# Kernel tuning notes

Measured on AMD Instinct MI355X. Metric: run time of the kernel, lower is better.

## Reference

```python
import jax, jax.numpy as jnp
import numpy as np

N = 50000   # nodes
E = 800000  # edges (avg degree 16)
F_IN = 128
H = 128
L = 4
LN_EPS = 1e-5


def setup_inputs() -> dict:
    key = jax.random.key(0)
    ks = jax.random.split(key, 4)
    x = jax.random.normal(ks[0], (N, F_IN), dtype=jnp.float32)
    edge_index = jax.random.randint(ks[1], (2, E), 0, N)
    conv_w = jax.random.normal(ks[2], (L, F_IN, H), dtype=jnp.float32) * 0.05
    conv_b = jnp.zeros((L, H), dtype=jnp.float32)
    ln_g = jnp.ones((L, H), dtype=jnp.float32)
    ln_b = jnp.zeros((L, H), dtype=jnp.float32)
    head_w = jax.random.normal(ks[3], (H, 1), dtype=jnp.float32) * 0.05
    head_b = jnp.zeros((1,), dtype=jnp.float32)
    return {"x": x, "edge_index": edge_index, "conv_w": conv_w, "conv_b": conv_b,
            "ln_g": ln_g, "ln_b": ln_b, "head_w": head_w, "head_b": head_b}


def _layer_norm(h, g, b):
    mu = jnp.mean(h, axis=-1, keepdims=True)
    var = jnp.mean(jnp.square(h - mu), axis=-1, keepdims=True)
    return (h - mu) * jax.lax.rsqrt(var + LN_EPS) * g + b


def _gcn_conv(h, W, b, src, dst, inv_sqrt_deg, inv_deg):
    # PyG GCNConv: self-loops + symmetric normalization D^-1/2 (A+I) D^-1/2, then bias.
    hw = h @ W  # (N, H)
    norm = inv_sqrt_deg[src] * inv_sqrt_deg[dst]  # (E,)
    msg = hw[src] * norm[:, None]  # gather + edgewise scale
    agg = jax.ops.segment_sum(msg, dst, num_segments=N)  # scatter-add
    agg = agg + hw * inv_deg[:, None]  # self-loop term (norm = 1/deg)
    return agg + b


def reference(x, edge_index, conv_w, conv_b, ln_g, ln_b, head_w, head_b):
    src, dst = edge_index[0], edge_index[1]
    # degree on target nodes, including self-loop
    deg = jax.ops.segment_sum(jnp.ones((E,), x.dtype), dst, num_segments=N) + 1.0
    inv_sqrt_deg = jax.lax.rsqrt(deg)
    inv_deg = 1.0 / deg
    h = x
    for i in range(L):
        h = _gcn_conv(h, conv_w[i], conv_b[i], src, dst, inv_sqrt_deg, inv_deg)
        h = _layer_norm(h, ln_g[i], ln_b[i])
        if i != L - 1:
            h = jax.nn.gelu(h, approximate=False)
            # dropout is identity in eval mode
    scores = (h @ head_w + head_b).squeeze(-1)  # (N,)
    return scores, h
```

## Files before the change

### kernel.cpp

```cpp
#include <hip/hip_runtime.h>
#include <math.h>

#define N_NODES 50000
#define N_EDGES 800000
#define HDIM 128
#define NLAYERS 4
#define LN_EPS 1e-5f
#define EQUARTER (N_EDGES / 4)
#define SEG 64
#define FILLB ((EQUARTER + 255) / 256)
#define GEMMB ((N_NODES + 63) / 64)

typedef __attribute__((ext_vector_type(8))) short short8;
typedef __attribute__((ext_vector_type(4))) float floatx4;

__device__ __forceinline__ ushort f2bf(float x) {
    unsigned b = __float_as_uint(x);
    unsigned r = b + 0x7fffu + ((b >> 16) & 1u);
    return (ushort)(r >> 16);
}
__device__ __forceinline__ float2 bf2f2(unsigned u) {
    return make_float2(__uint_as_float(u << 16), __uint_as_float(u & 0xffff0000u));
}


__device__ __forceinline__ void fill_body(int bid, int tid, const int* __restrict__ src,
                                          const int* __restrict__ dst, int* __restrict__ cnt,
                                          ushort* __restrict__ csr16) {
    int t = bid * 256 + tid;
    if (t >= EQUARTER) return;
    int s0 = src[t],                d0 = dst[t];
    int s1 = src[t + EQUARTER],     d1 = dst[t + EQUARTER];
    int s2 = src[t + 2 * EQUARTER], d2 = dst[t + 2 * EQUARTER];
    int s3 = src[t + 3 * EQUARTER], d3 = dst[t + 3 * EQUARTER];
    int p0 = atomicAdd(&cnt[d0], 1);
    int p1 = atomicAdd(&cnt[d1], 1);
    int p2 = atomicAdd(&cnt[d2], 1);
    int p3 = atomicAdd(&cnt[d3], 1);
    if (p0 < SEG) csr16[d0 * SEG + p0] = (ushort)s0;
    if (p1 < SEG) csr16[d1 * SEG + p1] = (ushort)s1;
    if (p2 < SEG) csr16[d2 * SEG + p2] = (ushort)s2;
    if (p3 < SEG) csr16[d3 * SEG + p3] = (ushort)s3;
}

__global__ __launch_bounds__(256) void isd_kernel(const int* __restrict__ cnt,
                                                  float* __restrict__ isd,
                                                  float* __restrict__ ind) {
    int i = blockIdx.x * 256 + threadIdx.x;
    if (i < N_NODES) {
        float d = (float)cnt[i] + 1.0f;
        isd[i] = rsqrtf(d);
        ind[i] = 1.0f / d;
    }
}

__global__ __launch_bounds__(256) void bprep_kernel(const float* __restrict__ W,
                                                    ushort* __restrict__ bfrag) {
    int idx = blockIdx.x * 256 + threadIdx.x;
    if (idx >= NLAYERS * 4 * 8 * 64) return;
    int lane = idx & 63;
    int t = (idx >> 6) & 7;
    int s = (idx >> 9) & 3;
    int l = idx >> 11;
    int n = t * 16 + (lane & 15);
    int kb = s * 32 + (lane >> 4) * 8;
    const float* Wl = W + (size_t)l * HDIM * HDIM;
    union { uint4 q; ushort u[8]; } o;
#pragma unroll
    for (int j = 0; j < 8; ++j) o.u[j] = f2bf(Wl[(size_t)(kb + j) * HDIM + n]);
    *(uint4*)&bfrag[(size_t)idx * 8] = o.q;
}

template <bool A_FP32>
__device__ __forceinline__ void gemm_body(int bid, int tid, const void* __restrict__ Av,
                                          const ushort* __restrict__ bfrag,
                                          ushort* __restrict__ out) {
    int wave = tid >> 6, lane = tid & 63;
    int quad = lane >> 4, mrow = lane & 15;
    int rowBase = bid * 64 + wave * 16;
    int arow = rowBase + mrow;
    bool aok = arow < N_NODES;

    floatx4 acc[8];
#pragma unroll
    for (int t = 0; t < 8; ++t) acc[t] = (floatx4)0.f;

#pragma unroll
    for (int s = 0; s < 4; ++s) {
        union { short8 v; ushort u[8]; } af;
        if (A_FP32) {
            const float* A = (const float*)Av;
            if (aok) {
                const float* p = &A[(size_t)arow * HDIM + s * 32 + quad * 8];
#pragma unroll
                for (int j = 0; j < 8; ++j) af.u[j] = f2bf(p[j]);
            } else {
#pragma unroll
                for (int j = 0; j < 8; ++j) af.u[j] = 0;
            }
        } else {
            const ushort* A = (const ushort*)Av;
            if (aok) {
                af.v = *(const short8*)&A[(size_t)arow * HDIM + s * 32 + quad * 8];
            } else {
#pragma unroll
                for (int j = 0; j < 8; ++j) af.u[j] = 0;
            }
        }
#pragma unroll
        for (int t = 0; t < 8; ++t) {
            short8 bf = *(const short8*)&bfrag[(size_t)(((s * 8 + t) * 64) + lane) * 8];
            acc[t] = __builtin_amdgcn_mfma_f32_16x16x32_bf16(af.v, bf, acc[t], 0, 0, 0);
        }
    }
#pragma unroll
    for (int t = 0; t < 8; ++t) {
#pragma unroll
        for (int r = 0; r < 4; ++r) {
            int row = rowBase + quad * 4 + r;
            if (row < N_NODES) out[(size_t)row * HDIM + t * 16 + mrow] = f2bf(acc[t][r]);
        }
    }
}

__global__ __launch_bounds__(256) void fused0_kernel(
    const int* __restrict__ src, const int* __restrict__ dst, int* __restrict__ cnt,
    ushort* __restrict__ csr16, const float* __restrict__ x,
    const ushort* __restrict__ bfrag0, ushort* __restrict__ hw) {
    if (blockIdx.x < FILLB)
        fill_body(blockIdx.x, threadIdx.x, src, dst, cnt, csr16);
    else
        gemm_body<true>(blockIdx.x - FILLB, threadIdx.x, x, bfrag0, hw);
}

__global__ __launch_bounds__(256) void gemm_mfma_kernel(const ushort* __restrict__ A,
                                                        const ushort* __restrict__ bfrag,
                                                        ushort* __restrict__ out) {
    gemm_body<false>(blockIdx.x, threadIdx.x, A, bfrag, out);
}

__global__ __launch_bounds__(256) void agg_ln_kernel(
    const uint2* __restrict__ hw2, const int* __restrict__ degcnt,
    const ushort* __restrict__ csr16, const float* __restrict__ isd,
    const float* __restrict__ ind, const float* __restrict__ conv_b,
    const float* __restrict__ ln_g, const float* __restrict__ ln_b,
    uint2* __restrict__ hout_bf, float* __restrict__ hout_f32,
    const float* __restrict__ head_w, const float* __restrict__ head_b,
    float* __restrict__ scores, int final_layer) {
    int wave = threadIdx.x >> 6;
    int lane = threadIdx.x & 63;
    int g = lane >> 5;
    int li = lane & 31;
    int n = blockIdx.x * 4 + wave;
    if (n >= N_NODES) return;
    int c = li * 4;

    float isd_n = isd[n], ind_n = ind[n];
    int rs = n * SEG;
    int deg = min(degcnt[n], SEG);

    float e0 = 0.f, e1 = 0.f, e2 = 0.f, e3 = 0.f;
    int sj = 0;
    float wj = 0.f;
    if (lane < deg) {
        sj = (int)csr16[rs + lane];
        wj = isd[sj];
    }
    for (int j = 0; j < deg; j += 8) {
#pragma unroll
        for (int t = 0; t < 4; ++t) {
            int idx = j + 2 * t + g;
            int s = __shfl(sj, idx);
            float w = __shfl(wj, idx);
            uint2 u = hw2[(size_t)s * 32 + li];
            float2 q0 = bf2f2(u.x), q1 = bf2f2(u.y);
            e0 = fmaf(q0.x, w, e0); e1 = fmaf(q0.y, w, e1);
            e2 = fmaf(q1.x, w, e2); e3 = fmaf(q1.y, w, e3);
        }
    }
    e0 += __shfl_xor(e0, 32); e1 += __shfl_xor(e1, 32);
    e2 += __shfl_xor(e2, 32); e3 += __shfl_xor(e3, 32);

    uint2 hv = hw2[(size_t)n * 32 + li];
    float2 h0 = bf2f2(hv.x), h1 = bf2f2(hv.y);
    float4 cb = *(const float4*)&conv_b[c];
    float a0 = fmaf(e0, isd_n, fmaf(h0.x, ind_n, cb.x));
    float a1 = fmaf(e1, isd_n, fmaf(h0.y, ind_n, cb.y));
    float a2 = fmaf(e2, isd_n, fmaf(h1.x, ind_n, cb.z));
    float a3 = fmaf(e3, isd_n, fmaf(h1.y, ind_n, cb.w));

    float sum = a0 + a1 + a2 + a3;
#pragma unroll
    for (int o = 1; o < 32; o <<= 1) sum += __shfl_xor(sum, o);
    float mu = sum * (1.0f / HDIM);
    float d0 = a0 - mu, d1 = a1 - mu, d2 = a2 - mu, d3 = a3 - mu;
    float vs = d0 * d0 + d1 * d1 + d2 * d2 + d3 * d3;
#pragma unroll
    for (int o = 1; o < 32; o <<= 1) vs += __shfl_xor(vs, o);
    float rstd = rsqrtf(vs * (1.0f / HDIM) + LN_EPS);
    float4 gv = *(const float4*)&ln_g[c];
    float4 bv = *(const float4*)&ln_b[c];
    float y0 = fmaf(d0 * rstd, gv.x, bv.x);
    float y1 = fmaf(d1 * rstd, gv.y, bv.y);
    float y2 = fmaf(d2 * rstd, gv.z, bv.z);
    float y3 = fmaf(d3 * rstd, gv.w, bv.w);

    if (!final_layer) {
#define GELU(v) ((v) = 0.5f * (v) * (1.0f + erff((v) * 0.70710678118654752f)))
        GELU(y0); GELU(y1); GELU(y2); GELU(y3);
#undef GELU
        if (g == 0) {
            uint2 ov;
            ov.x = (unsigned)f2bf(y0) | ((unsigned)f2bf(y1) << 16);
            ov.y = (unsigned)f2bf(y2) | ((unsigned)f2bf(y3) << 16);
            hout_bf[(size_t)n * 32 + li] = ov;
        }
    } else {
        if (g == 0)
            *(float4*)&hout_f32[(size_t)n * HDIM + c] = make_float4(y0, y1, y2, y3);
        float4 hwv = *(const float4*)&head_w[c];
        float p = y0 * hwv.x + y1 * hwv.y + y2 * hwv.z + y3 * hwv.w;
#pragma unroll
        for (int o = 1; o < 32; o <<= 1) p += __shfl_xor(p, o);
        if (lane == 0) scores[n] = p + head_b[0];
    }
}


extern "C" void kernel_launch(void* const* d_in, const int* in_sizes, int n_in,
                              void* d_out, int out_size, void* d_ws, size_t ws_size,
                              hipStream_t stream) {
    const float* x      = (const float*)d_in[0];
    const int*   eidx   = (const int*)d_in[1];
    const float* conv_w = (const float*)d_in[2];
    const float* conv_b = (const float*)d_in[3];
    const float* ln_g   = (const float*)d_in[4];
    const float* ln_b   = (const float*)d_in[5];
    const float* head_w = (const float*)d_in[6];
    const float* head_b = (const float*)d_in[7];
    float* out = (float*)d_out;

    const int* src = eidx;
    const int* dst = eidx + N_EDGES;

    char* ws = (char*)d_ws;
    size_t o = 0;
    auto alloc = [&](size_t elems) {
        void* p = ws + o * 4;
        o += (elems + 15) & ~(size_t)15;
        return p;
    };
    int*      cnt      = (int*)alloc(N_NODES);
    float*    isd      = (float*)alloc(N_NODES);
    float*    ind      = (float*)alloc(N_NODES);
    ushort*   csr16    = (ushort*)alloc((size_t)N_NODES * SEG / 2);
    ushort*   bfrag    = (ushort*)alloc(NLAYERS * 4 * 8 * 64 * 8 / 2);
    unsigned* hw       = (unsigned*)alloc((size_t)N_NODES * 64);
    unsigned* hbuf     = (unsigned*)alloc((size_t)N_NODES * 64);

    hipMemsetAsync(cnt, 0, N_NODES * sizeof(int), stream);
    bprep_kernel<<<(NLAYERS * 4 * 8 * 64 + 255) / 256, 256, 0, stream>>>(conv_w, bfrag);
    fused0_kernel<<<FILLB + GEMMB, 256, 0, stream>>>(src, dst, cnt, csr16, x, bfrag,
                                                     (ushort*)hw);
    isd_kernel<<<(N_NODES + 255) / 256, 256, 0, stream>>>(cnt, isd, ind);

    const unsigned* hin = hw;
    for (int l = 0; l < NLAYERS; ++l) {
        if (l > 0) {
            const ushort* bl = bfrag + (size_t)l * 4 * 8 * 64 * 8;
            gemm_mfma_kernel<<<GEMMB, 256, 0, stream>>>((const ushort*)hbuf, bl, (ushort*)hw);
        }
        int fin = (l == NLAYERS - 1) ? 1 : 0;
        agg_ln_kernel<<<(N_NODES + 3) / 4, 256, 0, stream>>>(
            (const uint2*)hw, cnt, csr16, isd, ind,
            conv_b + (size_t)l * HDIM, ln_g + (size_t)l * HDIM, ln_b + (size_t)l * HDIM,
            (uint2*)hbuf, out + N_NODES, head_w, head_b, out, fin);
    }
}
```

Before: 360.8 us.

## Fuse aggregation, GEMM and LayerNorm per layer by aggregating before projecting

```diff
diff --git a/kernel.cpp b/kernel.cpp
--- a/kernel.cpp
+++ b/kernel.cpp
@@ -133,12 +133,6 @@
         gemm_body<true>(blockIdx.x - FILLB, threadIdx.x, x, bfrag0, hw);
 }
 
-__global__ __launch_bounds__(256) void gemm_mfma_kernel(const ushort* __restrict__ A,
-                                                        const ushort* __restrict__ bfrag,
-                                                        ushort* __restrict__ out) {
-    gemm_body<false>(blockIdx.x, threadIdx.x, A, bfrag, out);
-}
-
 __global__ __launch_bounds__(256) void agg_ln_kernel(
     const uint2* __restrict__ hw2, const int* __restrict__ degcnt,
     const ushort* __restrict__ csr16, const float* __restrict__ isd,
@@ -226,6 +220,142 @@
     }
 }
 
+__global__ __launch_bounds__(256) void layer_fused_kernel(
+    const uint2* __restrict__ h2, const int* __restrict__ degcnt,
+    const ushort* __restrict__ csr16, const float* __restrict__ isd,
+    const float* __restrict__ ind, const ushort* __restrict__ bfrag,
+    const float* __restrict__ conv_b, const float* __restrict__ ln_g,
+    const float* __restrict__ ln_b, uint2* __restrict__ hout_bf,
+    float* __restrict__ hout_f32, const float* __restrict__ head_w,
+    const float* __restrict__ head_b, float* __restrict__ scores,
+    int final_layer) {
+    __shared__ float aggsf[64][132];
+    int wave = threadIdx.x >> 6, lane = threadIdx.x & 63;
+    int g = lane >> 5, li = lane & 31;
+
+    for (int it = 0; it < 16; ++it) {
+        int rblk = wave * 16 + it;
+        int n = blockIdx.x * 64 + rblk;
+        float a0 = 0.f, a1 = 0.f, a2 = 0.f, a3 = 0.f;
+        if (n < N_NODES) {
+            float isd_n = isd[n], ind_n = ind[n];
+            int rs = n * SEG;
+            int deg = min(degcnt[n], SEG);
+            float e0 = 0.f, e1 = 0.f, e2 = 0.f, e3 = 0.f;
+            int sj = 0;
+            float wj = 0.f;
+            if (lane < deg) {
+                sj = (int)csr16[rs + lane];
+                wj = isd[sj];
+            }
+            for (int j = 0; j < deg; j += 8) {
+#pragma unroll
+                for (int t = 0; t < 4; ++t) {
+                    int idx = j + 2 * t + g;
+                    int s = __shfl(sj, idx);
+                    float w = __shfl(wj, idx);
+                    uint2 u = h2[(size_t)s * 32 + li];
+                    float2 q0 = bf2f2(u.x), q1 = bf2f2(u.y);
+                    e0 = fmaf(q0.x, w, e0); e1 = fmaf(q0.y, w, e1);
+                    e2 = fmaf(q1.x, w, e2); e3 = fmaf(q1.y, w, e3);
+                }
+            }
+            e0 += __shfl_xor(e0, 32); e1 += __shfl_xor(e1, 32);
+            e2 += __shfl_xor(e2, 32); e3 += __shfl_xor(e3, 32);
+            uint2 hv = h2[(size_t)n * 32 + li];
+            float2 h0 = bf2f2(hv.x), h1v = bf2f2(hv.y);
+            a0 = fmaf(e0, isd_n, h0.x * ind_n);
+            a1 = fmaf(e1, isd_n, h0.y * ind_n);
+            a2 = fmaf(e2, isd_n, h1v.x * ind_n);
+            a3 = fmaf(e3, isd_n, h1v.y * ind_n);
+        }
+        if (g == 0)
+            *(float4*)&aggsf[rblk][li * 4] = make_float4(a0, a1, a2, a3);
+    }
+
+    int quad = lane >> 4, mrow = lane & 15;
+    floatx4 acc[8];
+#pragma unroll
+    for (int t = 0; t < 8; ++t) acc[t] = (floatx4)0.f;
+#pragma unroll
+    for (int s = 0; s < 4; ++s) {
+        const float* rowp = &aggsf[wave * 16 + mrow][s * 32 + quad * 8];
+        float4 pa = *(const float4*)rowp;
+        float4 pb = *(const float4*)(rowp + 4);
+        float p[8] = {pa.x, pa.y, pa.z, pa.w, pb.x, pb.y, pb.z, pb.w};
+        union { short8 v; ushort u[8]; } hi, lo;
+#pragma unroll
+        for (int j = 0; j < 8; ++j) {
+            ushort h = f2bf(p[j]);
+            hi.u[j] = h;
+            float hf = __uint_as_float((unsigned)h << 16);
+            lo.u[j] = f2bf(p[j] - hf);
+        }
+#pragma unroll
+        for (int t = 0; t < 8; ++t) {
+            short8 bf = *(const short8*)&bfrag[(size_t)(((s * 8 + t) * 64) + lane) * 8];
+            acc[t] = __builtin_amdgcn_mfma_f32_16x16x32_bf16(lo.v, bf, acc[t], 0, 0, 0);
+            acc[t] = __builtin_amdgcn_mfma_f32_16x16x32_bf16(hi.v, bf, acc[t], 0, 0, 0);
+        }
+    }
+
+    {
+        float cb[8];
+#pragma unroll
+        for (int t = 0; t < 8; ++t) cb[t] = conv_b[t * 16 + mrow];
+#pragma unroll
+        for (int t = 0; t < 8; ++t)
+#pragma unroll
+            for (int r = 0; r < 4; ++r)
+                aggsf[wave * 16 + quad * 4 + r][t * 16 + mrow] = acc[t][r] + cb[t];
+    }
+
+    int c = li * 4;
+    float4 gv = *(const float4*)&ln_g[c];
+    float4 bv = *(const float4*)&ln_b[c];
+    float4 hwv = *(const float4*)&head_w[c];
+    for (int it = 0; it < 16; ++it) {
+        int row = wave * 16 + it;
+        int n = blockIdx.x * 64 + row;
+        if (n >= N_NODES) continue;
+        float4 v = *(const float4*)&aggsf[row][c];
+        float a0 = v.x, a1 = v.y, a2 = v.z, a3 = v.w;
+
+        float sum = a0 + a1 + a2 + a3;
+#pragma unroll
+        for (int o = 1; o < 32; o <<= 1) sum += __shfl_xor(sum, o);
+        float mu = sum * (1.0f / HDIM);
+        float d0 = a0 - mu, d1 = a1 - mu, d2 = a2 - mu, d3 = a3 - mu;
+        float vs = d0 * d0 + d1 * d1 + d2 * d2 + d3 * d3;
+#pragma unroll
+        for (int o = 1; o < 32; o <<= 1) vs += __shfl_xor(vs, o);
+        float rstd = rsqrtf(vs * (1.0f / HDIM) + LN_EPS);
+        float y0 = fmaf(d0 * rstd, gv.x, bv.x);
+        float y1 = fmaf(d1 * rstd, gv.y, bv.y);
+        float y2 = fmaf(d2 * rstd, gv.z, bv.z);
+        float y3 = fmaf(d3 * rstd, gv.w, bv.w);
+
+        if (!final_layer) {
+#define GELU(v) ((v) = 0.5f * (v) * (1.0f + erff((v) * 0.70710678118654752f)))
+            GELU(y0); GELU(y1); GELU(y2); GELU(y3);
+#undef GELU
+            if (g == 0) {
+                uint2 ov;
+                ov.x = (unsigned)f2bf(y0) | ((unsigned)f2bf(y1) << 16);
+                ov.y = (unsigned)f2bf(y2) | ((unsigned)f2bf(y3) << 16);
+                hout_bf[(size_t)n * 32 + li] = ov;
+            }
+        } else {
+            if (g == 0)
+                *(float4*)&hout_f32[(size_t)n * HDIM + c] = make_float4(y0, y1, y2, y3);
+            float p = y0 * hwv.x + y1 * hwv.y + y2 * hwv.z + y3 * hwv.w;
+#pragma unroll
+            for (int o = 1; o < 32; o <<= 1) p += __shfl_xor(p, o);
+            if (lane == 0) scores[n] = p + head_b[0];
+        }
+    }
+}
+
 
 extern "C" void kernel_launch(void* const* d_in, const int* in_sizes, int n_in,
                               void* d_out, int out_size, void* d_ws, size_t ws_size,
@@ -264,16 +394,22 @@
                                                      (ushort*)hw);
     isd_kernel<<<(N_NODES + 255) / 256, 256, 0, stream>>>(cnt, isd, ind);
 
-    const unsigned* hin = hw;
-    for (int l = 0; l < NLAYERS; ++l) {
-        if (l > 0) {
-            const ushort* bl = bfrag + (size_t)l * 4 * 8 * 64 * 8;
-            gemm_mfma_kernel<<<GEMMB, 256, 0, stream>>>((const ushort*)hbuf, bl, (ushort*)hw);
-        }
+    agg_ln_kernel<<<(N_NODES + 3) / 4, 256, 0, stream>>>(
+        (const uint2*)hw, cnt, csr16, isd, ind,
+        conv_b, ln_g, ln_b,
+        (uint2*)hbuf, out + N_NODES, head_w, head_b, out, 0);
+
+    const unsigned* hin = hbuf;
+    unsigned* hnext = hw;
+    for (int l = 1; l < NLAYERS; ++l) {
+        const ushort* bl = bfrag + (size_t)l * 4 * 8 * 64 * 8;
         int fin = (l == NLAYERS - 1) ? 1 : 0;
-        agg_ln_kernel<<<(N_NODES + 3) / 4, 256, 0, stream>>>(
-            (const uint2*)hw, cnt, csr16, isd, ind,
+        layer_fused_kernel<<<GEMMB, 256, 0, stream>>>(
+            (const uint2*)hin, cnt, csr16, isd, ind, bl,
             conv_b + (size_t)l * HDIM, ln_g + (size_t)l * HDIM, ln_b + (size_t)l * HDIM,
-            (uint2*)hbuf, out + N_NODES, head_w, head_b, out, fin);
-    }
-}
+            (uint2*)hnext, out + N_NODES, head_w, head_b, out, fin);
+        const unsigned* tmp = hin;
+        hin = hnext;
+        hnext = (unsigned*)tmp;
+    }
+}
```

New measurement: 389.5 us. 7.9% more time.
